# Kernel optimization log

Measured on AMD Instinct MI355X. Metric: run time of the kernel, lower is better.

Reference implementation:

```python
import jax, jax.numpy as jnp
import numpy as np

DIM = 384
K = 10
LN_EPS = 1e-5


def sqdist(src, dst):
    # src [B,N,3], dst [B,M,3] -> [B,N,M] squared euclidean
    d = -2.0 * jnp.einsum('bnc,bmc->bnm', src, dst)
    d += jnp.sum(src ** 2, -1)[:, :, None]
    d += jnp.sum(dst ** 2, -1)[:, None, :]
    return d


def index_points(points, idx):
    # points [B,M,C], idx [B,...] int -> [B,...,C]
    B = points.shape[0]
    flat = idx.reshape(B, -1)
    out = jnp.take_along_axis(points, flat[..., None], axis=1)
    return out.reshape(idx.shape + (points.shape[-1],))


def setup_inputs() -> dict:
    key = jax.random.key(0)
    ks = jax.random.split(key, 10)
    B, N, C = 4, 2048, DIM
    inp = {
        'q': jax.random.normal(ks[0], (B, N, C), jnp.float32),
        'q_pos': jax.random.normal(ks[1], (B, N, 3), jnp.float32),
        # proj_v_off: Linear(dim, dim)
        'Wv': jax.random.normal(ks[2], (C, C), jnp.float32) * 0.02,
        'bv': jnp.zeros((C,), jnp.float32),
        # linear_offset: Linear(2*dim, dim) -> LayerNorm(dim) -> GELU -> Linear(dim, 3, bias=False)
        'W1': jax.random.normal(ks[3], (2 * C, C), jnp.float32) * 0.02,
        'b1': jnp.zeros((C,), jnp.float32),
        'ln_g': jnp.ones((C,), jnp.float32),
        'ln_b': jnp.zeros((C,), jnp.float32),
        'W2': jax.random.normal(ks[4], (C, 3), jnp.float32) * 0.02,
        # knn_map: Linear(2*dim, dim) -> LeakyReLU(0.2)
        'Wk': jax.random.normal(ks[5], (2 * C, C), jnp.float32) * 0.02,
        'bk': jnp.zeros((C,), jnp.float32),
    }
    return inp


def reference(q, q_pos, Wv, bv, W1, b1, ln_g, ln_b, W2, Wk, bk):
    B, N, C = q.shape
    # knn_point: k nearest v_pos for each q_pos (self-attn: v=q, v_pos=q_pos)
    neg_d, idx = jax.lax.top_k(-sqdist(q_pos, q_pos), K)          # idx [B,N,K]

    v_off = q @ Wv + bv                                           # [B,N,C]
    off_local_v = index_points(v_off, idx)                        # [B,N,K,C]
    qk = jnp.broadcast_to(q[:, :, None, :], (B, N, K, C))
    shift_feat = jnp.concatenate([off_local_v, qk], axis=-1)      # [B,N,K,2C]

    h = shift_feat @ W1 + b1
    mu = jnp.mean(h, -1, keepdims=True)
    var = jnp.mean((h - mu) ** 2, -1, keepdims=True)
    h = (h - mu) * jax.lax.rsqrt(var + LN_EPS) * ln_g + ln_b
    h = jax.nn.gelu(h, approximate=False)
    offset = jnp.tanh(h @ W2)                                     # [B,N,K,3]

    local_v_pos = index_points(q_pos, idx)                        # [B,N,K,3]
    scale = (jnp.max(local_v_pos, -2) - jnp.min(local_v_pos, -2))[:, :, None, :] * 0.5
    shift_pos = (local_v_pos + offset * scale).reshape(B, N * K, 3)

    # three_nn: 3 nearest v_pos per shifted point (squared dists, as pointnet2 CUDA)
    neg_d3, idx3 = jax.lax.top_k(-sqdist(shift_pos, q_pos), 3)    # [B,N*K,3]
    dist = -neg_d3
    recip = 1.0 / (dist + 1e-8)
    weight = recip / jnp.sum(recip, -1, keepdims=True)

    nb = index_points(q, idx3)                                    # [B,N*K,3,C]
    interp = jnp.sum(nb * weight[..., None], axis=-2)             # [B,N*K,C]
    interp = interp.reshape(B, N, K, C)

    feature = jnp.concatenate([interp - qk, qk], axis=-1)         # [B,N,K,2C]
    out = jax.nn.leaky_relu(feature @ Wk + bk, 0.2)               # [B,N,K,C]
    return jnp.max(out, axis=-2)                                  # [B,N,C]
```

## Files before the change

kernel.cpp:

```cpp
#include <hip/hip_runtime.h>
#include <hip/hip_bf16.h>
#include <math.h>

#define C_DIM 384
#define N_PTS 2048
#define K_NN 10
#define NK (N_PTS * K_NN)
#define LN_EPS_F 1e-5f

#define TCC 8
#define TCHUNK (N_PTS / TCC)

__device__ __forceinline__ float wave_sum64(float v) {
#pragma unroll
  for (int off = 32; off > 0; off >>= 1) v += __shfl_xor(v, off, 64);
  return v;
}

__device__ __forceinline__ unsigned long long shfl_xor_u64(unsigned long long v, int m) {
  return (unsigned long long)__shfl_xor((long long)v, m, 64);
}

#define BM 128
#define BN_T 128
#define BK 32
#define LDT 132

__global__ __launch_bounds__(256) void sgemm_q4_kernel(
    const float* __restrict__ A0, const float* __restrict__ A1,
    const float* __restrict__ A2, const float* __restrict__ A3,
    const float* __restrict__ B0, const float* __restrict__ B1,
    const float* __restrict__ B2, const float* __restrict__ B3,
    const float* __restrict__ bias0, const float* __restrict__ bias1,
    const float* __restrict__ bias2, const float* __restrict__ bias3,
    float* __restrict__ O0, float* __restrict__ O1,
    float* __restrict__ O2, float* __restrict__ O3) {
  __shared__ float As[BK][LDT];
  __shared__ float Bs[BK][LDT];
  const int bx = blockIdx.x;
  const int seg = bx / 3;
  const int n0 = (bx % 3) * BN_T;
  const int m0 = blockIdx.y * BM;
  const float* Ap = (seg == 0) ? A0 : (seg == 1) ? A1 : (seg == 2) ? A2 : A3;
  const float* Bp = (seg == 0) ? B0 : (seg == 1) ? B1 : (seg == 2) ? B2 : B3;
  const float* bp = (seg == 0) ? bias0 : (seg == 1) ? bias1 : (seg == 2) ? bias2 : bias3;
  float* Op = (seg == 0) ? O0 : (seg == 1) ? O1 : (seg == 2) ? O2 : O3;

  const int tid = threadIdx.x;
  const int tn = tid & 15;
  const int tm = tid >> 4;

  float acc[8][8] = {};
  for (int k0 = 0; k0 < C_DIM; k0 += BK) {
#pragma unroll
    for (int h = 0; h < 4; ++h) {
      const int r = (tid >> 3) + (h << 5);
      const int kc = (tid & 7) << 2;
      float4 a4 = *reinterpret_cast<const float4*>(
          &Ap[(size_t)(m0 + r) * C_DIM + k0 + kc]);
      As[kc + 0][r] = a4.x; As[kc + 1][r] = a4.y;
      As[kc + 2][r] = a4.z; As[kc + 3][r] = a4.w;
      const int brow = (tid >> 5) + (h << 3);
      const int bcol = (tid & 31) << 2;
      float4 b4 = *reinterpret_cast<const float4*>(
          &Bp[(size_t)(k0 + brow) * C_DIM + n0 + bcol]);
      *reinterpret_cast<float4*>(&Bs[brow][bcol]) = b4;
    }
    __syncthreads();
#pragma unroll
    for (int kk = 0; kk < BK; ++kk) {
      float4 a0 = *reinterpret_cast<const float4*>(&As[kk][tm << 3]);
      float4 a1 = *reinterpret_cast<const float4*>(&As[kk][(tm << 3) + 4]);
      float4 b0 = *reinterpret_cast<const float4*>(&Bs[kk][tn << 2]);
      float4 b1 = *reinterpret_cast<const float4*>(&Bs[kk][(tn << 2) + 64]);
      float av[8] = {a0.x, a0.y, a0.z, a0.w, a1.x, a1.y, a1.z, a1.w};
      float bw[8] = {b0.x, b0.y, b0.z, b0.w, b1.x, b1.y, b1.z, b1.w};
#pragma unroll
      for (int i = 0; i < 8; ++i)
#pragma unroll
        for (int j = 0; j < 8; ++j) acc[i][j] = fmaf(av[i], bw[j], acc[i][j]);
    }
    __syncthreads();
  }
#pragma unroll
  for (int i = 0; i < 8; ++i) {
    const int m = m0 + (tm << 3) + i;
    const int c0 = n0 + (tn << 2);
    float4 o0, o1;
    o0.x = acc[i][0]; o0.y = acc[i][1]; o0.z = acc[i][2]; o0.w = acc[i][3];
    o1.x = acc[i][4]; o1.y = acc[i][5]; o1.z = acc[i][6]; o1.w = acc[i][7];
    if (bp) {
      o0.x += bp[c0 + 0]; o0.y += bp[c0 + 1]; o0.z += bp[c0 + 2]; o0.w += bp[c0 + 3];
      o1.x += bp[c0 + 64]; o1.y += bp[c0 + 65]; o1.z += bp[c0 + 66]; o1.w += bp[c0 + 67];
    }
    *reinterpret_cast<float4*>(&Op[(size_t)m * C_DIM + c0]) = o0;
    *reinterpret_cast<float4*>(&Op[(size_t)m * C_DIM + c0 + 64]) = o1;
  }
}

__global__ __launch_bounds__(256) void gemm384_kernel(
    const float* __restrict__ A, const float* __restrict__ W,
    const float* __restrict__ bias, float* __restrict__ Out) {
  __shared__ float As[32][64];
  __shared__ float Bs[32][64];
  const int bm = blockIdx.y * 64;
  const int bn = blockIdx.x * 64;
  const int tid = threadIdx.x;
  const int tx = tid & 15;
  const int ty = tid >> 4;
  const int arow = tid >> 3;
  const int akc  = (tid & 7) << 2;
  const int brow = tid >> 4;
  const int bnc  = (tid & 15) << 2;
  float acc[4][4] = {{0.f, 0.f, 0.f, 0.f}, {0.f, 0.f, 0.f, 0.f},
                     {0.f, 0.f, 0.f, 0.f}, {0.f, 0.f, 0.f, 0.f}};
  for (int k0 = 0; k0 < C_DIM; k0 += 32) {
#pragma unroll
    for (int h = 0; h < 2; ++h) {
      float4 a4 = *reinterpret_cast<const float4*>(
          &A[(size_t)(bm + arow + h * 32) * C_DIM + k0 + akc]);
      As[akc + 0][arow + h * 32] = a4.x;
      As[akc + 1][arow + h * 32] = a4.y;
      As[akc + 2][arow + h * 32] = a4.z;
      As[akc + 3][arow + h * 32] = a4.w;
      float4 b4 = *reinterpret_cast<const float4*>(
          &W[(size_t)(k0 + brow + h * 16) * C_DIM + bn + bnc]);
      *reinterpret_cast<float4*>(&Bs[brow + h * 16][bnc]) = b4;
    }
    __syncthreads();
#pragma unroll
    for (int k = 0; k < 32; ++k) {
      float4 a4 = *reinterpret_cast<const float4*>(&As[k][ty << 2]);
      float4 b4 = *reinterpret_cast<const float4*>(&Bs[k][tx << 2]);
      float av[4] = {a4.x, a4.y, a4.z, a4.w};
      float bw[4] = {b4.x, b4.y, b4.z, b4.w};
#pragma unroll
      for (int i = 0; i < 4; ++i)
#pragma unroll
        for (int j = 0; j < 4; ++j) acc[i][j] = fmaf(av[i], bw[j], acc[i][j]);
    }
    __syncthreads();
  }
#pragma unroll
  for (int i = 0; i < 4; ++i) {
    const int m = bm + (ty << 2) + i;
    const int n0 = bn + (tx << 2);
    float4 o;
    o.x = acc[i][0]; o.y = acc[i][1]; o.z = acc[i][2]; o.w = acc[i][3];
    if (bias) {
      o.x += bias[n0 + 0]; o.y += bias[n0 + 1];
      o.z += bias[n0 + 2]; o.w += bias[n0 + 3];
    }
    *reinterpret_cast<float4*>(&Out[(size_t)m * C_DIM + n0]) = o;
  }
}

__global__ __launch_bounds__(256) void knn_wave_kernel(
    const float* __restrict__ q_pos, int* __restrict__ idx_out,
    float* __restrict__ scale_out) {
  const int wid = threadIdx.x >> 6;
  const int lane = threadIdx.x & 63;
  const int q = blockIdx.x * 4 + wid;
  const int b = q >> 11;
  const int qi = q & 2047;
  __shared__ float4 sc[N_PTS];
  const float* P = q_pos + (size_t)b * N_PTS * 3;
  for (int i = threadIdx.x; i < N_PTS; i += 256) {
    float x = P[i * 3 + 0], y = P[i * 3 + 1], z = P[i * 3 + 2];
    float s = __fadd_rn(__fadd_rn(__fmul_rn(x, x), __fmul_rn(y, y)), __fmul_rn(z, z));
    sc[i] = make_float4(x, y, z, s);
  }
  __syncthreads();
  const float4 qc = sc[qi];
  unsigned long long bd[K_NN];
#pragma unroll
  for (int t = 0; t < K_NN; ++t) bd[t] = ~0ull;
  for (int t = 0; t < N_PTS / 64; ++t) {
    const int j = (t << 6) + lane;
    float4 c = sc[j];
    float dot = __fadd_rn(__fadd_rn(__fmul_rn(qc.x, c.x), __fmul_rn(qc.y, c.y)),
                          __fmul_rn(qc.z, c.z));
    float d = __fadd_rn(__fadd_rn(__fmul_rn(-2.f, dot), qc.w), c.w);
    unsigned int db = __float_as_uint(d);
    db ^= (unsigned int)((int)db >> 31) | 0x80000000u;
    unsigned long long v = ((unsigned long long)db << 32) | (unsigned int)j;
    if (v < bd[K_NN - 1]) {
#pragma unroll
      for (int r = 0; r < K_NN; ++r) {
        bool lt = bd[r] < v;
        unsigned long long lo = lt ? bd[r] : v;
        unsigned long long hi = lt ? v : bd[r];
        bd[r] = lo; v = hi;
      }
    }
  }
  unsigned long long cur = bd[0];
  unsigned long long mine = 0;
#pragma unroll
  for (int r = 0; r < K_NN; ++r) {
    unsigned long long m = cur;
#pragma unroll
    for (int off = 32; off >= 1; off >>= 1) {
      unsigned long long o = shfl_xor_u64(m, off);
      m = (o < m) ? o : m;
    }
    if (cur == m) {
      cur = bd[1];
#pragma unroll
      for (int s = 1; s < K_NN - 1; ++s) bd[s] = bd[s + 1];
      bd[K_NN - 1] = ~0ull;
    }
    if (lane == r) mine = m;
  }
  const int nidx = (int)(mine & 0xFFFFFFFFull);
  if (lane < K_NN) idx_out[(size_t)q * K_NN + lane] = nidx;
  float mnx, mny, mnz, mxx, mxy, mxz;
  if (lane < K_NN) {
    float4 c = sc[nidx];
    mnx = c.x; mny = c.y; mnz = c.z; mxx = c.x; mxy = c.y; mxz = c.z;
  } else {
    mnx = 1e30f; mny = 1e30f; mnz = 1e30f;
    mxx = -1e30f; mxy = -1e30f; mxz = -1e30f;
  }
#pragma unroll
  for (int off = 32; off >= 1; off >>= 1) {
    mnx = fminf(mnx, __shfl_xor(mnx, off, 64));
    mny = fminf(mny, __shfl_xor(mny, off, 64));
    mnz = fminf(mnz, __shfl_xor(mnz, off, 64));
    mxx = fmaxf(mxx, __shfl_xor(mxx, off, 64));
    mxy = fmaxf(mxy, __shfl_xor(mxy, off, 64));
    mxz = fmaxf(mxz, __shfl_xor(mxz, off, 64));
  }
  if (lane == 0) {
    scale_out[(size_t)q * 3 + 0] = (mxx - mnx) * 0.5f;
    scale_out[(size_t)q * 3 + 1] = (mxy - mny) * 0.5f;
    scale_out[(size_t)q * 3 + 2] = (mxz - mnz) * 0.5f;
  }
}

__global__ __launch_bounds__(256) void mid_kernel(
    const float* __restrict__ hv, const float* __restrict__ hq,
    const int* __restrict__ idx, const float* __restrict__ scale,
    const float* __restrict__ q_pos, const float* __restrict__ ln_g,
    const float* __restrict__ ln_b, const float* __restrict__ W2,
    float* __restrict__ shift_pos) {
  const int wid = threadIdx.x >> 6;
  const int lane = threadIdx.x & 63;
  const long row = (long)blockIdx.x * 4 + wid;
  const long bn = row / K_NN;
  const int b = (int)(bn / N_PTS);
  const int g = idx[row];
  const float* hvp = hv + ((size_t)b * N_PTS + g) * C_DIM;
  const float* hqp = hq + (size_t)bn * C_DIM;
  float h[6];
  float s = 0.f;
#pragma unroll
  for (int r = 0; r < 6; ++r) {
    h[r] = hvp[lane + (r << 6)] + hqp[lane + (r << 6)];
    s += h[r];
  }
  s = wave_sum64(s);
  const float mu = s / 384.f;
  float hc[6];
  float vs = 0.f;
#pragma unroll
  for (int r = 0; r < 6; ++r) { hc[r] = h[r] - mu; vs += hc[r] * hc[r]; }
  vs = wave_sum64(vs);
  const float inv = 1.f / sqrtf(vs / 384.f + LN_EPS_F);
  float o0 = 0.f, o1 = 0.f, o2 = 0.f;
#pragma unroll
  for (int r = 0; r < 6; ++r) {
    const int c = lane + (r << 6);
    float y = hc[r] * inv * ln_g[c] + ln_b[c];
    float ge = 0.5f * y * (1.f + erff(y * 0.70710678118654752f));
    o0 += ge * W2[c * 3 + 0];
    o1 += ge * W2[c * 3 + 1];
    o2 += ge * W2[c * 3 + 2];
  }
  o0 = wave_sum64(o0); o1 = wave_sum64(o1); o2 = wave_sum64(o2);
  if (lane < 3) {
    float o = (lane == 0) ? o0 : ((lane == 1) ? o1 : o2);
    float off = tanhf(o);
    float lv = q_pos[((size_t)b * N_PTS + g) * 3 + lane];
    float sc = scale[(size_t)bn * 3 + lane];
    shift_pos[(size_t)row * 3 + lane] = lv + off * sc;
  }
}

__global__ __launch_bounds__(256) void three_nn_part_kernel(
    const float* __restrict__ shift_pos, const float* __restrict__ q_pos,
    float* __restrict__ pd3, int* __restrict__ pi3) {
  const int cc = blockIdx.x;
  const int qc = blockIdx.y;
  const int b = qc / (NK / 256);
  const float* P = q_pos + (size_t)b * N_PTS * 3;
  __shared__ float4 sc[TCHUNK];
  const int c0 = cc * TCHUNK;
  for (int i = threadIdx.x; i < TCHUNK; i += 256) {
    float x = P[(c0 + i) * 3 + 0], y = P[(c0 + i) * 3 + 1], z = P[(c0 + i) * 3 + 2];
    float s = __fadd_rn(__fadd_rn(__fmul_rn(x, x), __fmul_rn(y, y)), __fmul_rn(z, z));
    sc[i] = make_float4(x, y, z, s);
  }
  __syncthreads();
  const long jq = (long)qc * 256 + threadIdx.x;
  const float* S = shift_pos + (size_t)jq * 3;
  const float px = S[0], py = S[1], pz = S[2];
  const float ps = __fadd_rn(__fadd_rn(__fmul_rn(px, px), __fmul_rn(py, py)),
                             __fmul_rn(pz, pz));
  float d0 = 1e30f, d1 = 1e30f, d2 = 1e30f;
  int i0 = 0, i1 = 0, i2 = 0;
  for (int j = 0; j < TCHUNK; ++j) {
    float4 c = sc[j];
    float dot = __fadd_rn(__fadd_rn(__fmul_rn(px, c.x), __fmul_rn(py, c.y)),
                          __fmul_rn(pz, c.z));
    float d = __fadd_rn(__fadd_rn(__fmul_rn(-2.f, dot), ps), c.w);
    if (d < d2) {
      int j0 = c0 + j;
      if (d < d0)      { d2 = d1; i2 = i1; d1 = d0; i1 = i0; d0 = d; i0 = j0; }
      else if (d < d1) { d2 = d1; i2 = i1; d1 = d; i1 = j0; }
      else             { d2 = d; i2 = j0; }
    }
  }
  const size_t base = ((size_t)jq * TCC + cc) * 3;
  pd3[base + 0] = d0; pd3[base + 1] = d1; pd3[base + 2] = d2;
  pi3[base + 0] = i0; pi3[base + 1] = i1; pi3[base + 2] = i2;
}

__global__ __launch_bounds__(256) void three_nn_merge_kernel(
    const float* __restrict__ pd3, const int* __restrict__ pi3,
    int* __restrict__ idx3, float* __restrict__ w3) {
  const long jq = (long)blockIdx.x * 256 + threadIdx.x;
  float d0 = 1e30f, d1 = 1e30f, d2 = 1e30f;
  int i0 = 0, i1 = 0, i2 = 0;
  const size_t base = (size_t)jq * TCC * 3;
  for (int e = 0; e < TCC * 3; ++e) {
    float d = pd3[base + e];
    if (d < d2) {
      int j0 = pi3[base + e];
      if (d < d0)      { d2 = d1; i2 = i1; d1 = d0; i1 = i0; d0 = d; i0 = j0; }
      else if (d < d1) { d2 = d1; i2 = i1; d1 = d; i1 = j0; }
      else             { d2 = d; i2 = j0; }
    }
  }
  const float r0 = 1.f / (d0 + 1e-8f);
  const float r1 = 1.f / (d1 + 1e-8f);
  const float r2 = 1.f / (d2 + 1e-8f);
  const float rs = (r0 + r1) + r2;
  const size_t ob = (size_t)jq * 3;
  idx3[ob + 0] = i0; idx3[ob + 1] = i1; idx3[ob + 2] = i2;
  w3[ob + 0] = r0 / rs; w3[ob + 1] = r1 / rs; w3[ob + 2] = r2 / rs;
}

__global__ __launch_bounds__(256) void final_kernel(
    const float* __restrict__ qa, const float* __restrict__ qb,
    const int* __restrict__ idx3, const float* __restrict__ w3,
    float* __restrict__ out) {
  const int wid = threadIdx.x >> 6;
  const int lane = threadIdx.x & 63;
  const long bn = (long)blockIdx.x * 4 + wid;
  const int b = (int)(bn / N_PTS);
  const float* qaB = qa + (size_t)b * N_PTS * C_DIM;
  float base[6], mx[6];
#pragma unroll
  for (int r = 0; r < 6; ++r) {
    const size_t c = (size_t)bn * C_DIM + lane + (r << 6);
    base[r] = qb[c] - qa[c];
    mx[r] = -1e30f;
  }
  const size_t kb = (size_t)bn * K_NN * 3;
  for (int k = 0; k < K_NN; ++k) {
    const int a0 = idx3[kb + k * 3 + 0];
    const int a1 = idx3[kb + k * 3 + 1];
    const int a2 = idx3[kb + k * 3 + 2];
    const float w0 = w3[kb + k * 3 + 0];
    const float w1 = w3[kb + k * 3 + 1];
    const float w2c = w3[kb + k * 3 + 2];
    const float* p0 = qaB + (size_t)a0 * C_DIM;
    const float* p1 = qaB + (size_t)a1 * C_DIM;
    const float* p2 = qaB + (size_t)a2 * C_DIM;
#pragma unroll
    for (int r = 0; r < 6; ++r) {
      const int c = lane + (r << 6);
      float v = w0 * p0[c] + w1 * p1[c] + w2c * p2[c] + base[r];
      v = (v >= 0.f) ? v : 0.2f * v;
      mx[r] = fmaxf(mx[r], v);
    }
  }
#pragma unroll
  for (int r = 0; r < 6; ++r)
    out[(size_t)bn * C_DIM + lane + (r << 6)] = mx[r];
}

extern "C" void kernel_launch(void* const* d_in, const int* in_sizes, int n_in,
                              void* d_out, int out_size, void* d_ws, size_t ws_size,
                              hipStream_t stream) {
  const float* q     = (const float*)d_in[0];
  const float* q_pos = (const float*)d_in[1];
  const float* Wv    = (const float*)d_in[2];
  const float* bv    = (const float*)d_in[3];
  const float* W1    = (const float*)d_in[4];
  const float* b1    = (const float*)d_in[5];
  const float* ln_g  = (const float*)d_in[6];
  const float* ln_b  = (const float*)d_in[7];
  const float* W2    = (const float*)d_in[8];
  const float* Wk    = (const float*)d_in[9];
  const float* bk    = (const float*)d_in[10];
  float* out = (float*)d_out;

  const int BN = in_sizes[0] / C_DIM;

  const size_t BNC = (size_t)BN * C_DIM;
  float* ws = (float*)d_ws;
  float* bufA = ws;
  float* bufB = bufA + BNC;
  float* bufC = bufB + BNC;
  float* bufD = bufC + BNC;
  float* shift = bufD + BNC;
  float* scale = shift + (size_t)BN * K_NN * 3;
  float* w3    = scale + (size_t)BN * 3;
  int*   idx   = (int*)(w3 + (size_t)BN * K_NN * 3);
  int*   idx3  = idx + (size_t)BN * K_NN;

  float* v_off = out;

  float* pd3 = bufB;
  int*   pi3 = (int*)bufC;

  knn_wave_kernel<<<BN / 4, 256, 0, stream>>>(q_pos, idx, scale);
  sgemm_q4_kernel<<<dim3(12, BN / BM), 256, 0, stream>>>(
      q, q, q, q,
      Wv, W1 + (size_t)C_DIM * C_DIM, Wk, Wk + (size_t)C_DIM * C_DIM,
      bv, b1, nullptr, bk, v_off, bufC, bufA, bufD);
  gemm384_kernel<<<dim3(C_DIM / 64, BN / 64), 256, 0, stream>>>(v_off, W1, nullptr, bufB);
  mid_kernel<<<(BN * K_NN) / 4, 256, 0, stream>>>(bufB, bufC, idx, scale, q_pos,
                                                  ln_g, ln_b, W2, shift);
  three_nn_part_kernel<<<dim3(TCC, (BN * K_NN) / 256), 256, 0, stream>>>(
      shift, q_pos, pd3, pi3);
  three_nn_merge_kernel<<<(BN * K_NN) / 256, 256, 0, stream>>>(pd3, pi3, idx3, w3);
  final_kernel<<<BN / 4, 256, 0, stream>>>(bufA, bufD, idx3, w3, out);
}
```

Before: 369.3 us.

## Move Wk projections of q to bf16 MFMA kernel, keep fp32 SGEMM for others

Splits the four-way fused fp32 SGEMM. The two Wk halves (qa and qb) now run on a bf16 MFMA kernel fed by new q-to-bf16 and Wk-transpose conversion kernels, while the Wv and W1 projections stay on a smaller-tile fp32 SGEMM. The aim is to offload half the projection FLOPs onto matrix cores. In exchange it adds two extra launches and conversion traffic, and lowers the precision of the final-layer features to bf16, which may affect accuracy.

Result: faster. 355.6 us (median of 2 runs) (-3.7%).

```diff
diff --git a/kernel.cpp b/kernel.cpp
--- a/kernel.cpp
+++ b/kernel.cpp
@@ -11,6 +11,9 @@
 #define TCC 8
 #define TCHUNK (N_PTS / TCC)
 
+typedef __attribute__((ext_vector_type(8))) short short8v;
+typedef __attribute__((ext_vector_type(4))) float f32x4;
+
 __device__ __forceinline__ float wave_sum64(float v) {
 #pragma unroll
   for (int off = 32; off > 0; off >>= 1) v += __shfl_xor(v, off, 64);
@@ -21,70 +24,155 @@
   return (unsigned long long)__shfl_xor((long long)v, m, 64);
 }
 
-#define BM 128
-#define BN_T 128
-#define BK 32
-#define LDT 132
-
-__global__ __launch_bounds__(256) void sgemm_q4_kernel(
-    const float* __restrict__ A0, const float* __restrict__ A1,
-    const float* __restrict__ A2, const float* __restrict__ A3,
+__device__ __forceinline__ unsigned short f32_to_bf16_rne(float x) {
+  unsigned int u = __float_as_uint(x);
+  u += 0x7FFFu + ((u >> 16) & 1u);
+  return (unsigned short)(u >> 16);
+}
+
+__global__ __launch_bounds__(256) void conv_q_kernel(
+    const float* __restrict__ q, unsigned short* __restrict__ outp) {
+  const size_t i = ((size_t)blockIdx.x * 256 + threadIdx.x) * 4;
+  float4 v = *reinterpret_cast<const float4*>(&q[i]);
+  ushort4 o;
+  o.x = f32_to_bf16_rne(v.x); o.y = f32_to_bf16_rne(v.y);
+  o.z = f32_to_bf16_rne(v.z); o.w = f32_to_bf16_rne(v.w);
+  *reinterpret_cast<ushort4*>(&outp[i]) = o;
+}
+
+__global__ __launch_bounds__(256) void conv_wkT_kernel(
+    const float* __restrict__ Wk, unsigned short* __restrict__ Bt) {
+  __shared__ unsigned short tile[64][68];
+  const int k0 = blockIdx.x * 64;
+  const int sn = blockIdx.y;
+  const int s  = sn / 6;
+  const int n0 = (sn % 6) * 64;
+  const int t = threadIdx.x;
+  const int r = t >> 2;
+  const int cc = t & 3;
+#pragma unroll
+  for (int h = 0; h < 4; ++h) {
+    const int c = cc * 16 + h * 4;
+    float4 v = *reinterpret_cast<const float4*>(
+        &Wk[(size_t)(s * 384 + k0 + r) * C_DIM + n0 + c]);
+    tile[c + 0][r] = f32_to_bf16_rne(v.x);
+    tile[c + 1][r] = f32_to_bf16_rne(v.y);
+    tile[c + 2][r] = f32_to_bf16_rne(v.z);
+    tile[c + 3][r] = f32_to_bf16_rne(v.w);
+  }
+  __syncthreads();
+#pragma unroll
+  for (int h = 0; h < 4; ++h) {
+    const int col = cc * 16 + h * 4;
+    ushort4 o;
+    o.x = tile[r][col + 0]; o.y = tile[r][col + 1];
+    o.z = tile[r][col + 2]; o.w = tile[r][col + 3];
+    *reinterpret_cast<ushort4*>(
+        &Bt[(size_t)(s * 384 + n0 + r) * C_DIM + k0 + col]) = o;
+  }
+}
+
+__global__ __launch_bounds__(64) void mfma_qaqb_kernel(
+    const unsigned short* __restrict__ qbf, const unsigned short* __restrict__ Bt,
+    const float* __restrict__ bk, float* __restrict__ qa, float* __restrict__ qb) {
+  const int lane = threadIdx.x;
+  const int bx = blockIdx.x;
+  const int seg = bx / 6;
+  const int n0 = (bx % 6) * 64;
+  const int m0 = blockIdx.y * 64;
+  const unsigned short* Bs = Bt + (size_t)seg * C_DIM * C_DIM;
+  const int lm = lane & 15;
+  const int lk = (lane >> 4) * 8;
+  f32x4 acc[4][4] = {};
+#pragma unroll 2
+  for (int k0 = 0; k0 < C_DIM; k0 += 32) {
+    short8v a[4], b[4];
+#pragma unroll
+    for (int i = 0; i < 4; ++i)
+      a[i] = *reinterpret_cast<const short8v*>(
+          &qbf[(size_t)(m0 + i * 16 + lm) * C_DIM + k0 + lk]);
+#pragma unroll
+    for (int j = 0; j < 4; ++j)
+      b[j] = *reinterpret_cast<const short8v*>(
+          &Bs[(size_t)(n0 + j * 16 + lm) * C_DIM + k0 + lk]);
+#pragma unroll
+    for (int i = 0; i < 4; ++i)
+#pragma unroll
+      for (int j = 0; j < 4; ++j)
+        acc[i][j] = __builtin_amdgcn_mfma_f32_16x16x32_bf16(a[i], b[j], acc[i][j], 0, 0, 0);
+  }
+  const int rb = (lane >> 4) * 4;
+#pragma unroll
+  for (int i = 0; i < 4; ++i)
+#pragma unroll
+    for (int j = 0; j < 4; ++j) {
+      const int c = n0 + j * 16 + lm;
+#pragma unroll
+      for (int r = 0; r < 4; ++r) {
+        const int m = m0 + i * 16 + rb + r;
+        float v = acc[i][j][r];
+        if (seg == 0) qa[(size_t)m * C_DIM + c] = v;
+        else          qb[(size_t)m * C_DIM + c] = v + bk[c];
+      }
+    }
+}
+
+__global__ __launch_bounds__(256) void sgemm_q2_kernel(
+    const float* __restrict__ q,
     const float* __restrict__ B0, const float* __restrict__ B1,
-    const float* __restrict__ B2, const float* __restrict__ B3,
     const float* __restrict__ bias0, const float* __restrict__ bias1,
-    const float* __restrict__ bias2, const float* __restrict__ bias3,
-    float* __restrict__ O0, float* __restrict__ O1,
-    float* __restrict__ O2, float* __restrict__ O3) {
-  __shared__ float As[BK][LDT];
-  __shared__ float Bs[BK][LDT];
+    float* __restrict__ O0, float* __restrict__ O1) {
+  __shared__ float As[32][68];
+  __shared__ float Bs[32][132];
   const int bx = blockIdx.x;
   const int seg = bx / 3;
-  const int n0 = (bx % 3) * BN_T;
-  const int m0 = blockIdx.y * BM;
-  const float* Ap = (seg == 0) ? A0 : (seg == 1) ? A1 : (seg == 2) ? A2 : A3;
-  const float* Bp = (seg == 0) ? B0 : (seg == 1) ? B1 : (seg == 2) ? B2 : B3;
-  const float* bp = (seg == 0) ? bias0 : (seg == 1) ? bias1 : (seg == 2) ? bias2 : bias3;
-  float* Op = (seg == 0) ? O0 : (seg == 1) ? O1 : (seg == 2) ? O2 : O3;
-
+  const int n0 = (bx % 3) * 128;
+  const int m0 = blockIdx.y * 64;
+  const float* Bp = seg ? B1 : B0;
+  const float* bp = seg ? bias1 : bias0;
+  float* Op = seg ? O1 : O0;
   const int tid = threadIdx.x;
   const int tn = tid & 15;
   const int tm = tid >> 4;
-
-  float acc[8][8] = {};
-  for (int k0 = 0; k0 < C_DIM; k0 += BK) {
-#pragma unroll
-    for (int h = 0; h < 4; ++h) {
-      const int r = (tid >> 3) + (h << 5);
-      const int kc = (tid & 7) << 2;
+  float acc[4][8] = {};
+  for (int k0 = 0; k0 < C_DIM; k0 += 32) {
+#pragma unroll
+    for (int h = 0; h < 2; ++h) {
+      const int idx = tid + h * 256;
+      const int r = idx >> 3;
+      const int kc = (idx & 7) * 4;
       float4 a4 = *reinterpret_cast<const float4*>(
-          &Ap[(size_t)(m0 + r) * C_DIM + k0 + kc]);
+          &q[(size_t)(m0 + r) * C_DIM + k0 + kc]);
       As[kc + 0][r] = a4.x; As[kc + 1][r] = a4.y;
       As[kc + 2][r] = a4.z; As[kc + 3][r] = a4.w;
-      const int brow = (tid >> 5) + (h << 3);
-      const int bcol = (tid & 31) << 2;
+    }
+#pragma unroll
+    for (int h = 0; h < 4; ++h) {
+      const int idx = tid + h * 256;
+      const int br = idx >> 5;
+      const int bc = (idx & 31) * 4;
       float4 b4 = *reinterpret_cast<const float4*>(
-          &Bp[(size_t)(k0 + brow) * C_DIM + n0 + bcol]);
-      *reinterpret_cast<float4*>(&Bs[brow][bcol]) = b4;
+          &Bp[(size_t)(k0 + br) * C_DIM + n0 + bc]);
+      *reinterpret_cast<float4*>(&Bs[br][bc]) = b4;
     }
     __syncthreads();
 #pragma unroll
-    for (int kk = 0; kk < BK; ++kk) {
-      float4 a0 = *reinterpret_cast<const float4*>(&As[kk][tm << 3]);
-      float4 a1 = *reinterpret_cast<const float4*>(&As[kk][(tm << 3) + 4]);
+    for (int kk = 0; kk < 32; ++kk) {
+      float4 a4 = *reinterpret_cast<const float4*>(&As[kk][tm << 2]);
       float4 b0 = *reinterpret_cast<const float4*>(&Bs[kk][tn << 2]);
       float4 b1 = *reinterpret_cast<const float4*>(&Bs[kk][(tn << 2) + 64]);
-      float av[8] = {a0.x, a0.y, a0.z, a0.w, a1.x, a1.y, a1.z, a1.w};
+      float av[4] = {a4.x, a4.y, a4.z, a4.w};
       float bw[8] = {b0.x, b0.y, b0.z, b0.w, b1.x, b1.y, b1.z, b1.w};
 #pragma unroll
-      for (int i = 0; i < 8; ++i)
+      for (int i = 0; i < 4; ++i)
 #pragma unroll
         for (int j = 0; j < 8; ++j) acc[i][j] = fmaf(av[i], bw[j], acc[i][j]);
     }
     __syncthreads();
   }
 #pragma unroll
-  for (int i = 0; i < 8; ++i) {
-    const int m = m0 + (tm << 3) + i;
+  for (int i = 0; i < 4; ++i) {
+    const int m = m0 + (tm << 2) + i;
     const int c0 = n0 + (tn << 2);
     float4 o0, o1;
     o0.x = acc[i][0]; o0.y = acc[i][1]; o0.z = acc[i][2]; o0.w = acc[i][3];
@@ -422,15 +510,17 @@
   int*   idx3  = idx + (size_t)BN * K_NN;
 
   float* v_off = out;
-
+  unsigned short* qbf = (unsigned short*)bufB;
+  unsigned short* WkT = (unsigned short*)bufC;
   float* pd3 = bufB;
   int*   pi3 = (int*)bufC;
 
+  conv_q_kernel<<<(BN * C_DIM) / 1024, 256, 0, stream>>>(q, qbf);
+  conv_wkT_kernel<<<dim3(6, 12), 256, 0, stream>>>(Wk, WkT);
   knn_wave_kernel<<<BN / 4, 256, 0, stream>>>(q_pos, idx, scale);
-  sgemm_q4_kernel<<<dim3(12, BN / BM), 256, 0, stream>>>(
-      q, q, q, q,
-      Wv, W1 + (size_t)C_DIM * C_DIM, Wk, Wk + (size_t)C_DIM * C_DIM,
-      bv, b1, nullptr, bk, v_off, bufC, bufA, bufD);
+  mfma_qaqb_kernel<<<dim3(12, BN / 64), 64, 0, stream>>>(qbf, WkT, bk, bufA, bufD);
+  sgemm_q2_kernel<<<dim3(6, BN / 64), 256, 0, stream>>>(
+      q, Wv, W1 + (size_t)C_DIM * C_DIM, bv, b1, v_off, bufC);
   gemm384_kernel<<<dim3(C_DIM / 64, BN / 64), 256, 0, stream>>>(v_off, W1, nullptr, bufB);
   mid_kernel<<<(BN * K_NN) / 4, 256, 0, stream>>>(bufB, bufC, idx, scale, q_pos,
                                                   ln_g, ln_b, W2, shift);
```
